# Kernel tuning notes

Hardware: AMD Instinct MI355X
Metric: run time of the kernel (lower is better)

Reference implementation:

```python
import jax, jax.numpy as jnp
import numpy as np

EPS = 1e-6
T, B = 64, 16
IN_SIZE, OUT_SIZE = 256, 256
W_LEN, N_CELLS, R = 128, 256, 4
HID = 512
CTRL_IN = IN_SIZE + R * W_LEN                 # 768
WRITE_CH = 3 * W_LEN + 3 + R                  # 391: key, erase, write_vec, free gates, beta, alloc gate, write gate
READ_CH = R * (W_LEN + 4)                     # 528: per head key, beta, 3 read modes
SHARP_CH = 2 * R                              # 8: sharpness factors for forward/backward dists
CTRL_OUT = WRITE_CH + READ_CH + SHARP_CH      # 927
CLIP = 20.0

def oneplus(x):
    return jax.nn.softplus(x) + 1.0

def cosine_address(memory, keys, betas):
    # memory [b,n,w]; keys [b,h,w]; betas [b,h] -> softmax(beta * cos_sim) over cells [b,h,n]
    dots = jnp.einsum('bhw,bnw->bhn', keys, memory)
    nrm = jnp.linalg.norm(keys, axis=-1)[:, :, None] * jnp.linalg.norm(memory, axis=-1)[:, None, :]
    return jax.nn.softmax(dots / (nrm + EPS) * betas[:, :, None], axis=-1)

def allocation(usages):
    # DNC allocation weighting: sort usage ascending, a = (1-u)*cumprod(u) in sorted order, scatter back
    u = usages * (1.0 - EPS) + EPS
    order = jnp.argsort(u, axis=-1)
    su = jnp.take_along_axis(u, order, axis=-1)
    cp = jnp.cumprod(su, axis=-1)
    shifted = jnp.concatenate([jnp.ones_like(cp[..., :1]), cp[..., :-1]], axis=-1)
    scores = (1.0 - su) * shifted
    inv = jnp.argsort(order, axis=-1)
    return jnp.take_along_axis(scores, inv, axis=-1)

def sharpen(d, f):
    # power-sharpening with renormalization (DistSharpnessEnhancer)
    d = d + EPS
    d = d / jnp.max(d, axis=-1, keepdims=True)
    d = d ** f[..., None]
    return d / jnp.sum(d, axis=-1, keepdims=True)

def setup_inputs() -> dict:
    key = jax.random.key(0)
    ks = jax.random.split(key, 8)
    def lin(k, i, o):
        return (jax.random.normal(k, (i, o), jnp.float32) / np.sqrt(i)).astype(jnp.float32)
    return {
        'in_data': jax.random.normal(ks[0], (T, B, IN_SIZE), jnp.float32),
        'Wx': lin(ks[1], CTRL_IN, 4 * HID),
        'Wh': lin(ks[2], HID, 4 * HID),
        'b_lstm': jnp.zeros((4 * HID,), jnp.float32),
        'Wc': lin(ks[3], HID, CTRL_OUT),
        'bc': jnp.zeros((CTRL_OUT,), jnp.float32),
        'Wo': lin(ks[4], HID, OUT_SIZE),
        'bo': jnp.zeros((OUT_SIZE,), jnp.float32),
        'Wr': lin(ks[5], R * W_LEN, OUT_SIZE),
        'br': jnp.zeros((OUT_SIZE,), jnp.float32),
    }

def _dnc_forward(in_data, Wx, Wh, b_lstm, Wc, bc, Wo, bo, Wr, br):
    eye = jnp.eye(N_CELLS, dtype=in_data.dtype)

    def step(carry, x_t):
        mem, usages, link, prec, prev_w, prev_rd, prev_rdata, h, c = carry
        # controller (LSTM) on [input, prev read data]
        ctrl_in = jnp.concatenate([x_t, prev_rdata.reshape(B, -1)], axis=-1)
        gates = ctrl_in @ Wx + h @ Wh + b_lstm
        i_g, f_g, g_g, o_g = jnp.split(gates, 4, axis=-1)
        c = jax.nn.sigmoid(f_g) * c + jax.nn.sigmoid(i_g) * jnp.tanh(g_g)
        h = jax.nn.sigmoid(o_g) * jnp.tanh(c)
        controls = jnp.clip(h @ Wc + bc, -CLIP, CLIP)
        wc = controls[:, :WRITE_CH]
        rc = controls[:, WRITE_CH:WRITE_CH + READ_CH].reshape(B, R, W_LEN + 4)
        sc = controls[:, WRITE_CH + READ_CH:]
        # ---- write head ----
        w_key = wc[:, :W_LEN]
        erase = jax.nn.sigmoid(wc[:, W_LEN:2 * W_LEN])
        write_vec = wc[:, 2 * W_LEN:3 * W_LEN]
        free = jax.nn.sigmoid(wc[:, 3 * W_LEN:3 * W_LEN + R])
        w_beta = oneplus(wc[:, 3 * W_LEN + R])
        a_gate = jax.nn.sigmoid(wc[:, 3 * W_LEN + R + 1])[:, None]
        w_gate = jax.nn.sigmoid(wc[:, 3 * W_LEN + R + 2])[:, None]
        psi = jnp.prod(1.0 - free[:, :, None] * prev_rd, axis=1)            # retention [B,N]
        usages = (usages + prev_w - usages * prev_w) * psi
        alloc = allocation(usages)
        cw = cosine_address(mem, w_key[:, None, :], w_beta[:, None])[:, 0]
        w_dist = w_gate * (a_gate * alloc + (1.0 - a_gate) * cw)           # [B,N]
        # dealloc_content=True: memory decayed by retention psi before erase/write
        mem = mem * psi[:, :, None] * (1.0 - w_dist[:, :, None] * erase[:, None, :]) \
              + w_dist[:, :, None] * write_vec[:, None, :]
        # ---- temporal link matrix ----
        wi = w_dist[:, :, None]
        wj = w_dist[:, None, :]
        link = ((1.0 - wi - wj) * link + wi * prec[:, None, :]) * (1.0 - eye)
        prec = (1.0 - jnp.sum(w_dist, axis=-1, keepdims=True)) * prec + w_dist
        fwd = jnp.einsum('bij,bhj->bhi', link, prev_rd)                    # L w
        bwd = jnp.einsum('bji,bhj->bhi', link, prev_rd)                    # L^T w
        factors = oneplus(sc)
        fwd = sharpen(fwd, factors[:, :R])
        bwd = sharpen(bwd, factors[:, R:])
        # ---- read head ----
        r_keys = rc[..., :W_LEN]
        r_beta = oneplus(rc[..., W_LEN])
        modes = jax.nn.softmax(rc[..., W_LEN + 1:], axis=-1)               # [B,R,3] = (bwd, content, fwd)
        cr = cosine_address(mem, r_keys, r_beta)
        r_dist = modes[..., 0:1] * bwd + modes[..., 1:2] * cr + modes[..., 2:3] * fwd
        r_data = jnp.einsum('bhn,bnw->bhw', r_dist, mem)
        out = h @ Wo + bo + r_data.reshape(B, -1) @ Wr + br
        return (mem, usages, link, prec, w_dist, r_dist, r_data, h, c), out

    z = jnp.zeros
    carry0 = (z((B, N_CELLS, W_LEN)), z((B, N_CELLS)), z((B, N_CELLS, N_CELLS)),
              z((B, N_CELLS)), z((B, N_CELLS)), z((B, R, N_CELLS)),
              z((B, R, W_LEN)), z((B, HID)), z((B, HID)))
    _, outs = jax.lax.scan(step, carry0, in_data)
    return outs                                                            # [T,B,OUT_SIZE]

def reference(in_data, Wx, Wh, b_lstm, Wc, bc, Wo, bo, Wr, br):
    return _dnc_forward(in_data, Wx, Wh, b_lstm, Wc, bc, Wo, bo, Wr, br)
```

## Files before the change

kernel.cpp:

```cpp
#include <hip/hip_runtime.h>
#include <math.h>

#define NT   64
#define NB   16
#define OUTS 256
#define WL   128
#define NC   256
#define NR   4
#define HIDN 512
#define G4   2048
#define KTOT 1280
#define WCH  391
#define COUT 927
#define EPSF 1e-6f
#define NBLK 256
#define THR  512

#define O_WG    0
#define O_WCc   10272
#define O_WOc   12336
#define O_PRD   13360
#define O_USG   14384
#define O_PRC   14640
#define O_WDP   14896
#define O_COWN  15152
#define O_RED   15184
#define O_SCAL  17744
#define O_SCT   17776
#define O_UNI   17792
#define SH_FLOATS 38336

__device__ __forceinline__ float sigf(float x){ return 1.0f/(1.0f+expf(-x)); }
__device__ __forceinline__ float oneplusf(float x){ return fmaxf(x,0.0f)+log1pf(expf(-fabsf(x)))+1.0f; }

__device__ __forceinline__ float waveSum(float v){
#pragma unroll
  for(int o=32;o>0;o>>=1) v += __shfl_down(v,o,64);
  return v;
}
__device__ __forceinline__ float waveMax(float v){
#pragma unroll
  for(int o=32;o>0;o>>=1) v = fmaxf(v,__shfl_down(v,o,64));
  return v;
}

__device__ __forceinline__ void g_storef(float* p, float v){
  __hip_atomic_store(p, v, __ATOMIC_RELAXED, __HIP_MEMORY_SCOPE_AGENT);
}
__device__ __forceinline__ float2 g_loadf2(const float* p){
  unsigned long long v = __hip_atomic_load((const unsigned long long*)p, __ATOMIC_RELAXED, __HIP_MEMORY_SCOPE_AGENT);
  union{unsigned long long u; float2 f;} c; c.u=v; return c.f;
}

__device__ __forceinline__ void gbarH(int* bar, int b, int gp){
  __syncthreads();
  if (threadIdx.x == 0){
    asm volatile("s_waitcnt vmcnt(0) lgkmcnt(0)" ::: "memory");
    int prev = __hip_atomic_fetch_add(bar + b*32, 1, __ATOMIC_RELAXED, __HIP_MEMORY_SCOPE_AGENT);
    if (prev == 16*gp - 1){
      int p2 = __hip_atomic_fetch_add(bar + 1536, 1, __ATOMIC_RELAXED, __HIP_MEMORY_SCOPE_AGENT);
      if (p2 == 16*gp - 1)
        __hip_atomic_store(bar + 1568, gp, __ATOMIC_RELAXED, __HIP_MEMORY_SCOPE_AGENT);
    }
    while (__hip_atomic_load(bar + 1568, __ATOMIC_RELAXED, __HIP_MEMORY_SCOPE_AGENT) < gp)
      __builtin_amdgcn_s_sleep(1);
    asm volatile("" ::: "memory");
  }
  __syncthreads();
}
__device__ __forceinline__ void lbar(int* bar, int b, int lp){
  __syncthreads();
  if (threadIdx.x == 0){
    asm volatile("s_waitcnt vmcnt(0) lgkmcnt(0)" ::: "memory");
    int prev = __hip_atomic_fetch_add(bar + 512 + b*32, 1, __ATOMIC_RELAXED, __HIP_MEMORY_SCOPE_AGENT);
    if (prev == 16*lp - 1){
      __hip_atomic_store(bar + 1024 + b*32, lp, __ATOMIC_RELAXED, __HIP_MEMORY_SCOPE_AGENT);
    } else {
      while (__hip_atomic_load(bar + 1024 + b*32, __ATOMIC_RELAXED, __HIP_MEMORY_SCOPE_AGENT) < lp)
        __builtin_amdgcn_s_sleep(1);
    }
    asm volatile("" ::: "memory");
  }
  __syncthreads();
}

__global__ void k_zero(float* p, size_t n){
  size_t i = (size_t)blockIdx.x*blockDim.x + threadIdx.x;
  size_t st = (size_t)gridDim.x*blockDim.x;
  for(; i<n; i+=st) p[i]=0.0f;
}

__global__ __launch_bounds__(THR,1) void k_persist(
    const float* __restrict__ Wx, const float* __restrict__ Wh, const float* __restrict__ b_lstm,
    const float* __restrict__ Wc, const float* __restrict__ bc,
    const float* __restrict__ Wo, const float* __restrict__ bo,
    const float* __restrict__ Wr, const float* __restrict__ br,
    const float* __restrict__ in_data,
    float* mem_g, float* linkT_g, float* racc_rot, float* h_rot, float* ctrl_rot,
    float* dots_g, float* bwd_g, float* facc_g, float* rlog_g,
    float* out_g, int* bar)
{
  extern __shared__ float SH[];
  float* s_wg   = SH + O_WG;
  float* s_wc   = SH + O_WCc;
  float* s_wo   = SH + O_WOc;
  float* s_prd  = SH + O_PRD;
  float* s_usage= SH + O_USG;
  float* s_prec = SH + O_PRC;
  float* s_wdp  = SH + O_WDP;
  float* s_cown = SH + O_COWN;
  float* s_red  = SH + O_RED;
  float* s_scal = SH + O_SCAL;
  float* s_sct  = SH + O_SCT;
  float* s_act  = SH + O_UNI;
  float* s_ctrl = SH + O_UNI;
  float* s_psi  = SH + O_UNI + 928;
  float* s_su   = SH + O_UNI + 1184;
  float* s_shift= SH + O_UNI + 1440;
  float* s_er   = SH + O_UNI + 1696;
  float* s_mn   = SH + O_UNI + 1824;
  float* s_preo = SH + O_UNI + 1840;
  float* s_link = SH + O_UNI + 1856;
  float* s_mem  = SH + O_UNI + 5952;
  float* s_fwd  = SH + O_UNI + 8000;
  float* s_bwd  = SH + O_UNI + 9024;
  float* s_rkey = SH + O_UNI + 10048;

  const int tid = threadIdx.x, bk = blockIdx.x;
  const int s = bk & 15, b = bk >> 4;

  for(int i=tid;i<10240;i+=THR){
    int c=i&7, k=i>>3;
    int col=(c>>1)*512 + 2*bk + (c&1);
    s_wg[c*1284+k] = (k<768) ? Wx[(size_t)k*G4+col] : Wh[(size_t)(k-768)*G4+col];
  }
  for(int i=tid;i<2048;i+=THR){
    int cl=i&3, k=i>>2;
    int j=4*bk+cl;
    s_wc[cl*516+k] = (bk<232 && j<COUT) ? Wc[(size_t)k*COUT+j] : 0.f;
  }
  for(int i=tid;i<1024;i+=THR){
    s_wo[i] = (i<512) ? Wr[(size_t)i*OUTS+bk] : Wo[(size_t)(i-512)*OUTS+bk];
  }
  for(int i=tid;i<1024;i+=THR) s_prd[i]=0.f;
  for(int i=tid;i<256;i+=THR){ s_usage[i]=0.f; s_prec[i]=0.f; s_wdp[i]=0.f; }
  if(tid<32) s_cown[tid]=0.f;
  __syncthreads();

  int myrk=0; float allocv=0.f;

  for(int t=0;t<=NT;t++){
    if(t<NT){
      for(int i=tid;i<2048;i+=THR){
        int bi=i>>7, k2=(i&127)*2;
        float2 v = *(const float2*)(in_data + (size_t)t*4096 + bi*256 + k2);
        s_act[bi*1284+k2]=v.x; s_act[bi*1284+k2+1]=v.y;
      }
    }
    for(int i=tid;i<4096;i+=THR){
      int bi=i>>8, k2=(i&255)*2;
      float2 v = *(const float2*)(racc_rot + (size_t)t*8192 + bi*512 + k2);
      s_act[bi*1284+256+k2]=v.x; s_act[bi*1284+256+k2+1]=v.y;
    }
    for(int i=tid;i<4096;i+=THR){
      int bi=i>>8, k2=(i&255)*2;
      float2 v = *(const float2*)(h_rot + (size_t)t*8192 + bi*512 + k2);
      s_act[bi*1284+768+k2]=v.x; s_act[bi*1284+768+k2+1]=v.y;
    }
    if(tid<64) g_storef(facc_g + b*1024 + s*64 + tid, 0.0f);
    __syncthreads();
    if(t<NT){
      int oc=tid&127, q=tid>>7; int c=oc>>4, bi=oc&15;
      const float* ap = s_act + bi*1284;
      const float* wp = s_wg + c*1284;
      float4 a4={0,0,0,0};
      int k0=q*320;
#pragma unroll 8
      for(int it=0;it<80;it++){
        int k=k0+it*4;
        float4 a=*(const float4*)(ap+k);
        float4 w=*(const float4*)(wp+k);
        a4.x+=a.x*w.x; a4.y+=a.y*w.y; a4.z+=a.z*w.z; a4.w+=a.w*w.w;
      }
      s_red[q*128+oc]=a4.x+a4.y+a4.z+a4.w;
    }
    if(t>0){
      int bi=tid>>5, q=tid&31;
      const float* ap = s_act + bi*1284 + 256;
      float acc=0.f;
#pragma unroll 8
      for(int it=0;it<32;it++){
        int k2=q+it*32;
        acc += ap[k2]*s_wo[k2];
      }
      s_red[512 + bi*32 + q] = acc;
    }
    __syncthreads();
    if(t<NT && tid<32){
      int j2=tid>>4, bi=tid&15;
      float g4[4];
#pragma unroll
      for(int g=0;g<4;g++){
        int c=g*2+j2;
        float v = s_red[0*128+c*16+bi]+s_red[1*128+c*16+bi]+s_red[2*128+c*16+bi]+s_red[3*128+c*16+bi];
        v += b_lstm[g*512 + 2*bk + j2];
        g4[g]=v;
      }
      float cc = sigf(g4[1])*s_cown[j2*16+bi] + sigf(g4[0])*tanhf(g4[2]);
      float hh = sigf(g4[3])*tanhf(cc);
      s_cown[j2*16+bi]=cc;
      g_storef(h_rot + (size_t)(t+1)*8192 + bi*512 + 2*bk + j2, hh);
    }
    if(t>0 && tid>=64 && tid<80){
      int bi=tid-64;
      float acc=bo[bk]+br[bk];
#pragma unroll
      for(int q=0;q<32;q++) acc += s_red[512+bi*32+q];
      out_g[((size_t)(t-1)*NB+bi)*OUTS + bk] = acc;
    }
    if(t==NT) break;
    gbarH(bar,b,3*t+1);

    for(int i=tid;i<4096;i+=THR){
      int bi=i>>8, k2=(i&255)*2;
      float2 v = *(const float2*)(h_rot + (size_t)(t+1)*8192 + bi*512 + k2);
      s_act[bi*1284+768+k2]=v.x; s_act[bi*1284+768+k2+1]=v.y;
    }
    __syncthreads();
    if(bk<232){
      int o=tid&63, ks=tid>>6; int cl=o>>4, bi=o&15;
      int j=4*bk+cl;
      float acc=0.f;
      if(j<COUT){
        const float* ap=s_act+bi*1284+768;
        const float* wp=s_wc+cl*516;
#pragma unroll
        for(int kk=0;kk<16;kk++){
          int k=ks*64+kk*4;
          float4 a=*(const float4*)(ap+k);
          float4 w=*(const float4*)(wp+k);
          acc += a.x*w.x+a.y*w.y+a.z*w.z+a.w*w.w;
        }
      }
      s_red[ks*64+o]=acc;
    }
    __syncthreads();
    if(bk<232 && tid<64){
      int cl=tid>>4, bi=tid&15; int j=4*bk+cl;
      if(j<COUT){
        float a=bc[j];
#pragma unroll
        for(int ks=0;ks<8;ks++) a+=s_red[ks*64+tid];
        g_storef(ctrl_rot + (size_t)t*14848 + bi*928 + j, fminf(fmaxf(a,-20.f),20.f));
      }
    }
    gbarH(bar,b,3*t+2);

    for(int i=tid;i<464;i+=THR){
      float2 v = *(const float2*)(ctrl_rot + (size_t)t*14848 + b*928 + 2*i);
      s_ctrl[2*i]=v.x; s_ctrl[2*i+1]=v.y;
    }
    __syncthreads();
    for(int i=tid;i<528;i+=THR) s_rkey[i]=s_ctrl[WCH+i];
    if(tid<256){
      int n=tid;
      float psi=1.f;
#pragma unroll
      for(int r=0;r<NR;r++) psi *= 1.f - sigf(s_ctrl[384+r])*s_prd[r*256+n];
      s_psi[n]=psi;
      float uo=s_usage[n], pw=s_wdp[n];
      s_usage[n]=(uo+pw-uo*pw)*psi;
    } else if(tid<384){
      int w=tid-256; s_er[w]=sigf(s_ctrl[128+w]);
    } else if(tid>=448){
      int l=tid-448;
      float v=s_ctrl[l]*s_ctrl[l]+s_ctrl[l+64]*s_ctrl[l+64];
      v=waveSum(v);
      if(l==0) s_scal[0]=v;
    }
    __syncthreads();
    {
      int n=tid&255, hf=tid>>8;
      float u2=s_usage[n]*(1.f-EPSF)+EPSF; int c=0;
      for(int jj=0;jj<128;jj++){
        int j=hf*128+jj;
        float uj=s_usage[j]*(1.f-EPSF)+EPSF;
        c += (uj<u2)||(uj==u2 && j<n);
      }
      s_red[hf*256+n]=(float)c;
    }
    __syncthreads();
    if(tid<256){
      myrk=(int)(s_red[tid]+s_red[256+tid]);
      s_su[myrk]=s_usage[tid]*(1.f-EPSF)+EPSF;
    }
    __syncthreads();
    if(tid<16){
      float run=1.f;
#pragma unroll
      for(int i=0;i<16;i++){ int idx=tid*16+i; s_shift[idx]=run; run*=s_su[idx]; }
      s_sct[tid]=run;
    }
    __syncthreads();
    if(tid==0){
      float run=1.f;
      for(int j=0;j<16;j++){ float t2=s_sct[j]; s_sct[j]=run; run*=t2; }
    }
    __syncthreads();
    if(tid<256) allocv=(1.f-s_su[myrk])*s_shift[myrk]*s_sct[myrk>>4];
    {
      int nr=tid>>5, wq=tid&31;
      int n=s*16+nr;
      float4 m=((const float4*)(mem_g + ((size_t)(b*256+n))*WL))[wq];
      int w=wq*4;
      float4 kk=*(const float4*)(s_ctrl+w);
      float dt=m.x*kk.x+m.y*kk.y+m.z*kk.z+m.w*kk.w;
      float m2=m.x*m.x+m.y*m.y+m.z*m.z+m.w*m.w;
      s_red[nr*32+wq]=dt; s_red[512+nr*32+wq]=m2;
    }
    __syncthreads();
    if(tid<16){
      float dt=0,m2=0;
#pragma unroll
      for(int q=0;q<32;q++){ dt+=s_red[tid*32+q]; m2+=s_red[512+tid*32+q]; }
      float wb=oneplusf(s_ctrl[388]);
      float lg=dt*wb/(sqrtf(s_scal[0])*sqrtf(m2)+EPSF);
      g_storef(dots_g+b*256+s*16+tid, lg);
    }
    lbar(bar,b,2*t+1);

    if(tid<128){
      float2 v=g_loadf2(dots_g+b*256+2*tid);
      s_red[2*tid]=v.x; s_red[2*tid+1]=v.y;
    }
    __syncthreads();
    {
      float lv=s_red[tid&255];
      float mv=waveMax(lv);
      if((tid&63)==0) s_scal[8+(tid>>6)]=mv;
      __syncthreads();
      float mx=s_scal[8]; for(int i=9;i<16;i++) mx=fmaxf(mx,s_scal[i]);
      float ex=expf(lv-mx);
      float sv=waveSum(ex);
      __syncthreads();
      if((tid&63)==0) s_scal[8+(tid>>6)]=sv;
      __syncthreads();
      float se=0; for(int i=8;i<16;i++) se+=s_scal[i]; se*=0.5f;
      if(tid<256){
        float cw=ex/se;
        float ag=sigf(s_ctrl[389]), wg=sigf(s_ctrl[390]);
        s_wdp[tid]=wg*(ag*allocv+(1.f-ag)*cw);
      }
    }
    __syncthreads();
    {
      float wv=waveSum(s_wdp[tid&255]);
      if((tid&63)==0) s_scal[8+(tid>>6)]=wv;
      __syncthreads();
      float swd=0; for(int i=8;i<16;i++) swd+=s_scal[i]; swd*=0.5f;
      if(tid<16) s_preo[tid]=s_prec[s*16+tid];
      __syncthreads();
      if(tid<256) s_prec[tid]=(1.f-swd)*s_prec[tid]+s_wdp[tid];
    }
    __syncthreads();
    {
      int nr=tid>>5, ic=tid&31;
      int n=s*16+nr;
      float wdn=s_wdp[n], pre=s_preo[nr];
      float4* lp=(float4*)(linkT_g+((size_t)(b*256+n))*256);
#pragma unroll
      for(int h2=0;h2<2;h2++){
        int i4=h2*32+ic;
        float4 l=lp[i4];
        int i0=i4*4;
        float4 wv=*(float4*)&s_wdp[i0];
        float4 nl;
        nl.x=(i0  ==n)?0.f:((1.f-wv.x-wdn)*l.x+wv.x*pre);
        nl.y=(i0+1==n)?0.f:((1.f-wv.y-wdn)*l.y+wv.y*pre);
        nl.z=(i0+2==n)?0.f:((1.f-wv.z-wdn)*l.z+wv.z*pre);
        nl.w=(i0+3==n)?0.f:((1.f-wv.w-wdn)*l.w+wv.w*pre);
        lp[i4]=nl;
        *(float4*)&s_link[nr*256+i0]=nl;
      }
    }
    __syncthreads();
    {
      int nr=tid>>5, ic=tid&31;
      float b0=0,b1=0,b2=0,b3=0;
#pragma unroll
      for(int q=0;q<8;q++){
        int i=q*32+ic;
        float l=s_link[nr*256+i];
        b0+=l*s_prd[i]; b1+=l*s_prd[256+i]; b2+=l*s_prd[512+i]; b3+=l*s_prd[768+i];
      }
      s_red[(0*16+nr)*32+ic]=b0; s_red[(1*16+nr)*32+ic]=b1;
      s_red[(2*16+nr)*32+ic]=b2; s_red[(3*16+nr)*32+ic]=b3;
    }
    __syncthreads();
    if(tid<64){
      int r=tid>>4, nr=tid&15;
      float a=0;
#pragma unroll
      for(int q=0;q<32;q++) a+=s_red[(r*16+nr)*32+q];
      g_storef(bwd_g + b*1024 + r*256 + s*16+nr, a);
    }
    {
      int np=tid&255, dh=tid>>8;
      float f0=0,f1=0;
#pragma unroll
      for(int jr=0;jr<16;jr++){
        float l=s_link[jr*256+np];
        int j=s*16+jr;
        f0+=l*s_prd[(2*dh)*256+j];
        f1+=l*s_prd[(2*dh+1)*256+j];
      }
      atomicAdd(facc_g + b*1024 + (2*dh)*256 + np, f0);
      atomicAdd(facc_g + b*1024 + (2*dh+1)*256 + np, f1);
    }
    {
      int nr=tid>>5, wq=tid&31;
      int n=s*16+nr;
      float ps=s_psi[n], wdn=s_wdp[n];
      float4* mr=(float4*)(mem_g+((size_t)(b*256+n))*WL);
      float4 m=mr[wq]; int w=wq*4;
      float4 er=*(const float4*)(s_er+w);
      float4 wv=*(const float4*)(s_ctrl+256+w);
      m.x=m.x*ps*(1.f-wdn*er.x)+wdn*wv.x;
      m.y=m.y*ps*(1.f-wdn*er.y)+wdn*wv.y;
      m.z=m.z*ps*(1.f-wdn*er.z)+wdn*wv.z;
      m.w=m.w*ps*(1.f-wdn*er.w)+wdn*wv.w;
      mr[wq]=m;
      *(float4*)&s_mem[nr*128+w]=m;
    }
    __syncthreads();
    {
      int nr=tid>>5, wq=tid&31;
      float4 m=*(float4*)&s_mem[nr*128+wq*4];
      int w=wq*4;
      float4 k0=*(const float4*)(s_rkey+w);
      float4 k1=*(const float4*)(s_rkey+132+w);
      float4 k2=*(const float4*)(s_rkey+264+w);
      float4 k3=*(const float4*)(s_rkey+396+w);
      float d0=m.x*k0.x+m.y*k0.y+m.z*k0.z+m.w*k0.w;
      float d1=m.x*k1.x+m.y*k1.y+m.z*k1.z+m.w*k1.w;
      float d2=m.x*k2.x+m.y*k2.y+m.z*k2.z+m.w*k2.w;
      float d3=m.x*k3.x+m.y*k3.y+m.z*k3.z+m.w*k3.w;
      float m2=m.x*m.x+m.y*m.y+m.z*m.z+m.w*m.w;
      s_red[(0*16+nr)*32+wq]=d0; s_red[(1*16+nr)*32+wq]=d1;
      s_red[(2*16+nr)*32+wq]=d2; s_red[(3*16+nr)*32+wq]=d3;
      s_red[2048+nr*32+wq]=m2;
    }
    if(tid<256){
      int r=tid>>6, l=tid&63;
      const float* kk=s_rkey+r*132;
      float kv=kk[l]*kk[l]+kk[l+64]*kk[l+64];
      kv=waveSum(kv);
      if(l==0) s_scal[4+r]=sqrtf(kv);
    }
    __syncthreads();
    if(tid<16){
      float m2=0;
#pragma unroll
      for(int q=0;q<32;q++) m2+=s_red[2048+tid*32+q];
      s_mn[tid]=sqrtf(m2);
    }
    __syncthreads();
    if(tid<64){
      int r=tid>>4, nr=tid&15;
      float dt=0;
#pragma unroll
      for(int q=0;q<32;q++) dt+=s_red[(r*16+nr)*32+q];
      float rb=oneplusf(s_rkey[r*132+128]);
      float lg=dt*rb/(s_scal[4+r]*s_mn[nr]+EPSF);
      g_storef(rlog_g+b*1024+r*256+s*16+nr,lg);
    }
    lbar(bar,b,2*t+2);

    {
      float2 v=g_loadf2(facc_g + b*1024 + 2*tid);
      s_fwd[2*tid]=v.x; s_fwd[2*tid+1]=v.y;
    }
    {
      float2 v=g_loadf2(bwd_g+b*1024+2*tid);
      s_bwd[2*tid]=v.x; s_bwd[2*tid+1]=v.y;
    }
    {
      float2 v=g_loadf2(rlog_g+b*1024+2*tid);
      s_red[2*tid]=v.x; s_red[2*tid+1]=v.y;
    }
    __syncthreads();
    {
      int l=tid&63, w=tid>>6;
      float* rp=(w<4)? (s_fwd+w*256) : (s_bwd+(w-4)*256);
      float a=rp[l]+EPSF, b2=rp[l+64]+EPSF, c2=rp[l+128]+EPSF, d2=rp[l+192]+EPSF;
      float mxr=waveMax(fmaxf(fmaxf(a,b2),fmaxf(c2,d2)));
      mxr=__shfl(mxr,0,64);
      float ff=oneplusf(s_ctrl[919+w]);
      a=powf(a/mxr,ff); b2=powf(b2/mxr,ff); c2=powf(c2/mxr,ff); d2=powf(d2/mxr,ff);
      float sm=waveSum(a+b2+c2+d2);
      sm=__shfl(sm,0,64);
      float inv=1.f/sm;
      rp[l]=a*inv; rp[l+64]=b2*inv; rp[l+128]=c2*inv; rp[l+192]=d2*inv;
    }
    {
      int l=tid&63, w=tid>>6, row=w&3;
      float* rr=s_red+row*256;
      float a=rr[l],b2=rr[l+64],c2=rr[l+128],d2=rr[l+192];
      float mx2=waveMax(fmaxf(fmaxf(a,b2),fmaxf(c2,d2)));
      mx2=__shfl(mx2,0,64);
      a=expf(a-mx2); b2=expf(b2-mx2); c2=expf(c2-mx2); d2=expf(d2-mx2);
      float sm=waveSum(a+b2+c2+d2);
      sm=__shfl(sm,0,64);
      float inv=1.f/sm;
      rr[l]=a*inv; rr[l+64]=b2*inv; rr[l+128]=c2*inv; rr[l+192]=d2*inv;
    }
    __syncthreads();
    if(tid<256){
      int n=tid;
#pragma unroll
      for(int r=0;r<NR;r++){
        float cr=s_red[r*256+n];
        float fw=s_fwd[r*256+n];
        float bw=s_bwd[r*256+n];
        int mo=WCH+r*132+129;
        float m0=s_ctrl[mo],m1=s_ctrl[mo+1],m2s=s_ctrl[mo+2];
        float mm=fmaxf(m0,fmaxf(m1,m2s));
        float e0=expf(m0-mm),e1=expf(m1-mm),e2=expf(m2s-mm);
        float es=e0+e1+e2;
        s_prd[r*256+n]=(e0*bw+e1*cr+e2*fw)/es;
      }
    }
    __syncthreads();
    {
      int w=tid&127, nq=tid>>7;
      float a0=0,a1=0,a2=0,a3=0;
#pragma unroll
      for(int q=0;q<4;q++){
        int nr=nq*4+q; int n=s*16+nr;
        float mv=s_mem[nr*128+w];
        a0+=s_prd[n]*mv; a1+=s_prd[256+n]*mv; a2+=s_prd[512+n]*mv; a3+=s_prd[768+n]*mv;
      }
      s_red[(0*4+nq)*128+w]=a0; s_red[(1*4+nq)*128+w]=a1;
      s_red[(2*4+nq)*128+w]=a2; s_red[(3*4+nq)*128+w]=a3;
    }
    __syncthreads();
    {
      int r=tid>>7, w=tid&127;
      float rd=s_red[(r*4+0)*128+w]+s_red[(r*4+1)*128+w]+s_red[(r*4+2)*128+w]+s_red[(r*4+3)*128+w];
      atomicAdd(racc_rot + (size_t)(t+1)*8192 + b*512 + r*128 + w, rd);
    }
    gbarH(bar,b,3*t+3);
  }
}

extern "C" void kernel_launch(void* const* d_in, const int* in_sizes, int n_in,
                              void* d_out, int out_size, void* d_ws, size_t ws_size,
                              hipStream_t stream) {
  const float* in_data = (const float*)d_in[0];
  const float* Wx      = (const float*)d_in[1];
  const float* Wh      = (const float*)d_in[2];
  const float* b_lstm  = (const float*)d_in[3];
  const float* Wc      = (const float*)d_in[4];
  const float* bc      = (const float*)d_in[5];
  const float* Wo      = (const float*)d_in[6];
  const float* bo      = (const float*)d_in[7];
  const float* Wr      = (const float*)d_in[8];
  const float* br      = (const float*)d_in[9];
  float* out = (float*)d_out;
  float* ws  = (float*)d_ws;

  size_t off=0;
  float* mem_     = ws+off; off += (size_t)NB*NC*WL;
  float* linkT_   = ws+off; off += (size_t)NB*NC*NC;
  float* racc_rot = ws+off; off += (size_t)65*8192;
  float* h_rot    = ws+off; off += (size_t)65*8192;
  float* ctrl_rot = ws+off; off += (size_t)64*14848;
  float* dots_    = ws+off; off += NB*NC;
  float* bwd_     = ws+off; off += NB*NR*NC;
  float* facc_    = ws+off; off += NB*NR*NC;
  float* rlog_    = ws+off; off += NB*NR*NC;
  int*   bar_     = (int*)(ws+off); off += 2048;
  size_t zero_floats = off;

  static const size_t SH_BYTES = (size_t)SH_FLOATS*sizeof(float);
  hipFuncSetAttribute((const void*)k_persist,
                      hipFuncAttributeMaxDynamicSharedMemorySize, (int)SH_BYTES);

  k_zero<<<256,256,0,stream>>>(ws, zero_floats);
  k_persist<<<NBLK,THR,SH_BYTES,stream>>>(Wx,Wh,b_lstm,Wc,bc,Wo,bo,Wr,br,in_data,
                                          mem_,linkT_,racc_rot,h_rot,ctrl_rot,
                                          dots_,bwd_,facc_,rlog_,out,bar_);
}
```

Before: 2.807 ms.

## Replace atomic-counter grid barriers with per-block flag barriers and widen loads

Swaps the fetch-add counter barriers for flag-based barriers. Each block stores a monotonically increasing phase value to its own slot, and 16 lanes poll the group's flags in parallel. The global barrier becomes hierarchical: block 0 of each group gathers its group and then publishes a group flag, which all blocks poll. The aim is to cut atomic contention and serialized round trips on the barrier, which runs several times per timestep across 256 blocks. Activation staging moves from float2 to float4 loads, and a redundant duplicated softmax done by the extra waves is removed.

```diff
diff --git a/kernel.cpp b/kernel.cpp
--- a/kernel.cpp
+++ b/kernel.cpp
@@ -52,31 +52,40 @@
   union{unsigned long long u; float2 f;} c; c.u=v; return c.f;
 }
 
-__device__ __forceinline__ void gbarH(int* bar, int b, int gp){
+__device__ __forceinline__ void bar_local(int* flagA, int b, int s, int pc){
   __syncthreads();
-  if (threadIdx.x == 0){
-    asm volatile("s_waitcnt vmcnt(0) lgkmcnt(0)" ::: "memory");
-    int prev = __hip_atomic_fetch_add(bar + b*32, 1, __ATOMIC_RELAXED, __HIP_MEMORY_SCOPE_AGENT);
-    if (prev == 16*gp - 1){
-      int p2 = __hip_atomic_fetch_add(bar + 1536, 1, __ATOMIC_RELAXED, __HIP_MEMORY_SCOPE_AGENT);
-      if (p2 == 16*gp - 1)
-        __hip_atomic_store(bar + 1568, gp, __ATOMIC_RELAXED, __HIP_MEMORY_SCOPE_AGENT);
-    }
-    while (__hip_atomic_load(bar + 1568, __ATOMIC_RELAXED, __HIP_MEMORY_SCOPE_AGENT) < gp)
-      __builtin_amdgcn_s_sleep(1);
+  if (threadIdx.x < 64){
+    int l = threadIdx.x;
+    if (l == 0){
+      asm volatile("s_waitcnt vmcnt(0) lgkmcnt(0)" ::: "memory");
+      __hip_atomic_store(flagA + b*16 + s, pc, __ATOMIC_RELAXED, __HIP_MEMORY_SCOPE_AGENT);
+    }
+    if (l < 16){
+      while (__hip_atomic_load(flagA + b*16 + l, __ATOMIC_RELAXED, __HIP_MEMORY_SCOPE_AGENT) < pc)
+        __builtin_amdgcn_s_sleep(1);
+    }
     asm volatile("" ::: "memory");
   }
   __syncthreads();
 }
-__device__ __forceinline__ void lbar(int* bar, int b, int lp){
+__device__ __forceinline__ void bar_global(int* flagA, int* flagB, int b, int s, int pc){
   __syncthreads();
-  if (threadIdx.x == 0){
-    asm volatile("s_waitcnt vmcnt(0) lgkmcnt(0)" ::: "memory");
-    int prev = __hip_atomic_fetch_add(bar + 512 + b*32, 1, __ATOMIC_RELAXED, __HIP_MEMORY_SCOPE_AGENT);
-    if (prev == 16*lp - 1){
-      __hip_atomic_store(bar + 1024 + b*32, lp, __ATOMIC_RELAXED, __HIP_MEMORY_SCOPE_AGENT);
-    } else {
-      while (__hip_atomic_load(bar + 1024 + b*32, __ATOMIC_RELAXED, __HIP_MEMORY_SCOPE_AGENT) < lp)
+  if (threadIdx.x < 64){
+    int l = threadIdx.x;
+    if (l == 0){
+      asm volatile("s_waitcnt vmcnt(0) lgkmcnt(0)" ::: "memory");
+      __hip_atomic_store(flagA + b*16 + s, pc, __ATOMIC_RELAXED, __HIP_MEMORY_SCOPE_AGENT);
+    }
+    if (s == 0){
+      if (l < 16){
+        while (__hip_atomic_load(flagA + b*16 + l, __ATOMIC_RELAXED, __HIP_MEMORY_SCOPE_AGENT) < pc)
+          __builtin_amdgcn_s_sleep(1);
+      }
+      if (l == 0)
+        __hip_atomic_store(flagB + b, pc, __ATOMIC_RELAXED, __HIP_MEMORY_SCOPE_AGENT);
+    }
+    if (l < 16){
+      while (__hip_atomic_load(flagB + l, __ATOMIC_RELAXED, __HIP_MEMORY_SCOPE_AGENT) < pc)
         __builtin_amdgcn_s_sleep(1);
     }
     asm volatile("" ::: "memory");
@@ -128,6 +137,9 @@
 
   const int tid = threadIdx.x, bk = blockIdx.x;
   const int s = bk & 15, b = bk >> 4;
+  int* flagA = bar;
+  int* flagB = bar + 256;
+  int pc = 0;
 
   for(int i=tid;i<10240;i+=THR){
     int c=i&7, k=i>>3;
@@ -151,26 +163,27 @@
 
   for(int t=0;t<=NT;t++){
     if(t<NT){
-      for(int i=tid;i<2048;i+=THR){
-        int bi=i>>7, k2=(i&127)*2;
-        float2 v = *(const float2*)(in_data + (size_t)t*4096 + bi*256 + k2);
-        s_act[bi*1284+k2]=v.x; s_act[bi*1284+k2+1]=v.y;
-      }
-    }
-    for(int i=tid;i<4096;i+=THR){
-      int bi=i>>8, k2=(i&255)*2;
-      float2 v = *(const float2*)(racc_rot + (size_t)t*8192 + bi*512 + k2);
-      s_act[bi*1284+256+k2]=v.x; s_act[bi*1284+256+k2+1]=v.y;
-    }
-    for(int i=tid;i<4096;i+=THR){
-      int bi=i>>8, k2=(i&255)*2;
-      float2 v = *(const float2*)(h_rot + (size_t)t*8192 + bi*512 + k2);
-      s_act[bi*1284+768+k2]=v.x; s_act[bi*1284+768+k2+1]=v.y;
+      for(int i=tid;i<1024;i+=THR){
+        int bi=i>>6, k4=(i&63)*4;
+        float4 v = *(const float4*)(in_data + (size_t)t*4096 + bi*256 + k4);
+        *(float4*)&s_act[bi*1284+k4] = v;
+      }
+    }
+    for(int i=tid;i<2048;i+=THR){
+      int bi=i>>7, k4=(i&127)*4;
+      float4 v = *(const float4*)(racc_rot + (size_t)t*8192 + bi*512 + k4);
+      *(float4*)&s_act[bi*1284+256+k4] = v;
+    }
+    for(int i=tid;i<2048;i+=THR){
+      int bi=i>>7, k4=(i&127)*4;
+      float4 v = *(const float4*)(h_rot + (size_t)t*8192 + bi*512 + k4);
+      *(float4*)&s_act[bi*1284+768+k4] = v;
     }
     if(tid<64) g_storef(facc_g + b*1024 + s*64 + tid, 0.0f);
     __syncthreads();
     if(t<NT){
-      int oc=tid&127, q=tid>>7; int c=oc>>4, bi=oc&15;
+      int oc=tid&127, q=tid>>7;
+      int c=oc>>4, bi=oc&15;
       const float* ap = s_act + bi*1284;
       const float* wp = s_wg + c*1284;
       float4 a4={0,0,0,0};
@@ -202,7 +215,9 @@
 #pragma unroll
       for(int g=0;g<4;g++){
         int c=g*2+j2;
-        float v = s_red[0*128+c*16+bi]+s_red[1*128+c*16+bi]+s_red[2*128+c*16+bi]+s_red[3*128+c*16+bi];
+        float v=0.f;
+#pragma unroll
+        for(int q=0;q<4;q++) v += s_red[q*128+c*16+bi];
         v += b_lstm[g*512 + 2*bk + j2];
         g4[g]=v;
       }
@@ -219,16 +234,17 @@
       out_g[((size_t)(t-1)*NB+bi)*OUTS + bk] = acc;
     }
     if(t==NT) break;
-    gbarH(bar,b,3*t+1);
-
-    for(int i=tid;i<4096;i+=THR){
-      int bi=i>>8, k2=(i&255)*2;
-      float2 v = *(const float2*)(h_rot + (size_t)(t+1)*8192 + bi*512 + k2);
-      s_act[bi*1284+768+k2]=v.x; s_act[bi*1284+768+k2+1]=v.y;
+    bar_global(flagA,flagB,b,s,++pc);
+
+    for(int i=tid;i<2048;i+=THR){
+      int bi=i>>7, k4=(i&127)*4;
+      float4 v = *(const float4*)(h_rot + (size_t)(t+1)*8192 + bi*512 + k4);
+      *(float4*)&s_act[bi*1284+768+k4] = v;
     }
     __syncthreads();
     if(bk<232){
-      int o=tid&63, ks=tid>>6; int cl=o>>4, bi=o&15;
+      int o=tid&63, ks=tid>>6;
+      int cl=o>>4, bi=o&15;
       int j=4*bk+cl;
       float acc=0.f;
       if(j<COUT){
@@ -254,11 +270,11 @@
         g_storef(ctrl_rot + (size_t)t*14848 + bi*928 + j, fminf(fmaxf(a,-20.f),20.f));
       }
     }
-    gbarH(bar,b,3*t+2);
-
-    for(int i=tid;i<464;i+=THR){
-      float2 v = *(const float2*)(ctrl_rot + (size_t)t*14848 + b*928 + 2*i);
-      s_ctrl[2*i]=v.x; s_ctrl[2*i+1]=v.y;
+    bar_global(flagA,flagB,b,s,++pc);
+
+    for(int i=tid;i<232;i+=THR){
+      float4 v = *(const float4*)(ctrl_rot + (size_t)t*14848 + b*928 + 4*i);
+      *(float4*)&s_ctrl[4*i] = v;
     }
     __syncthreads();
     for(int i=tid;i<528;i+=THR) s_rkey[i]=s_ctrl[WCH+i];
@@ -327,7 +343,7 @@
       float lg=dt*wb/(sqrtf(s_scal[0])*sqrtf(m2)+EPSF);
       g_storef(dots_g+b*256+s*16+tid, lg);
     }
-    lbar(bar,b,2*t+1);
+    bar_local(flagA,b,s,++pc);
 
     if(tid<128){
       float2 v=g_loadf2(dots_g+b*256+2*tid);
@@ -474,7 +490,7 @@
       float lg=dt*rb/(s_scal[4+r]*s_mn[nr]+EPSF);
       g_storef(rlog_g+b*1024+r*256+s*16+nr,lg);
     }
-    lbar(bar,b,2*t+2);
+    bar_local(flagA,b,s,++pc);
 
     {
       float2 v=g_loadf2(facc_g + b*1024 + 2*tid);
@@ -502,9 +518,9 @@
       float inv=1.f/sm;
       rp[l]=a*inv; rp[l+64]=b2*inv; rp[l+128]=c2*inv; rp[l+192]=d2*inv;
     }
-    {
-      int l=tid&63, w=tid>>6, row=w&3;
-      float* rr=s_red+row*256;
+    if(tid<256){
+      int l=tid&63, w=tid>>6;
+      float* rr=s_red+w*256;
       float a=rr[l],b2=rr[l+64],c2=rr[l+128],d2=rr[l+192];
       float mx2=waveMax(fmaxf(fmaxf(a,b2),fmaxf(c2,d2)));
       mx2=__shfl(mx2,0,64);
@@ -549,7 +565,7 @@
       float rd=s_red[(r*4+0)*128+w]+s_red[(r*4+1)*128+w]+s_red[(r*4+2)*128+w]+s_red[(r*4+3)*128+w];
       atomicAdd(racc_rot + (size_t)(t+1)*8192 + b*512 + r*128 + w, rd);
     }
-    gbarH(bar,b,3*t+3);
+    bar_global(flagA,flagB,b,s,++pc);
   }
 }
 
```

Result: slower. 3.006 ms (+7.1%).
